# Optimization experiments

Measured on AMD Instinct MI355X. Metric: run time of the kernel, lower is better.

Reference implementation:

```python
import jax, jax.numpy as jnp
import numpy as np

LOG2 = 0.6931471805599453

def ssp(x):
    # shifted softplus: softplus(x) - log(2)
    return jax.nn.softplus(x) - LOG2

def residual(v, W, b):
    # PhysNetResidual reuses the same linear twice: linear(act(linear(act(x)))) + x
    h = ssp(v) @ W + b
    h = ssp(h) @ W + b
    return h + v

def setup_inputs() -> dict:
    key = jax.random.key(0)
    ks = jax.random.split(key, 20)
    N, E, D, R = 50000, 600000, 128, 32
    n_int, n_atom_res, n_out_res = 3, 1, 1
    def orth(k, shape):
        return jax.random.orthogonal(k, shape[0])[: shape[0], : shape[1]].astype(jnp.float32) if shape[0] == shape[1] else jax.random.normal(k, shape, jnp.float32) * (1.0 / np.sqrt(shape[0]))
    return {
        "x": jax.random.normal(ks[0], (N, D), jnp.float32),
        "g_ij": jax.random.uniform(ks[1], (E, R), jnp.float32),
        "Wf": orth(ks[2], (D, D)), "bf": jnp.zeros((D,), jnp.float32),
        "Wg": jax.random.normal(ks[3], (R, D), jnp.float32) * (1.0 / np.sqrt(R)),
        "Wj": orth(ks[4], (D, D)), "bj": jnp.zeros((D,), jnp.float32),
        "Wi": orth(ks[5], (D, D)), "bi": jnp.zeros((D,), jnp.float32),
        "u": jnp.ones((D,), jnp.float32),
        "rWint": jnp.stack([orth(ks[6 + i], (D, D)) for i in range(n_int)]),
        "rbint": jnp.zeros((n_int, D), jnp.float32),
        "rWatom": jnp.stack([orth(ks[10 + i], (D, D)) for i in range(n_atom_res)]),
        "rbatom": jnp.zeros((n_atom_res, D), jnp.float32),
        "rWout": jnp.stack([orth(ks[12 + i], (D, D)) for i in range(n_out_res)]),
        "rbout": jnp.zeros((n_out_res, D), jnp.float32),
        "idx_i": jax.random.randint(ks[14], (E,), 0, N, jnp.int32),
        "idx_j": jax.random.randint(ks[15], (E,), 0, N, jnp.int32),
        "n_atoms": N,
    }

def reference(x, g_ij, Wf, bf, Wg, Wj, bj, Wi, bi, u,
              rWint, rbint, rWatom, rbatom, rWout, rbout,
              idx_i, idx_j, n_atoms):
    # --- PhysNetInteraction ---
    xa = ssp(x)                                   # [N, D]
    x_j = xa[idx_j]                               # gather -> [E, D]
    xp = u * xa                                   # [N, D]
    vp = ssp(x_j @ Wj + bj) * (g_ij @ Wg)         # [E, D] RBF-gated messages
    vm = ssp(xa @ Wi + bi)                        # [N, D]
    v = jax.ops.segment_sum(vp, idx_i, num_segments=n_atoms) + vm
    for k in range(rWint.shape[0]):
        v = residual(v, rWint[k], rbint[k])
    v = ssp(v)
    h = xp + v @ Wf + bf                          # [N, D]
    # --- atomic residual stack ---
    for k in range(rWatom.shape[0]):
        h = residual(h, rWatom[k], rbatom[k])
    # --- PhysNetOutput ---
    o = h
    for k in range(rWout.shape[0]):
        o = residual(o, rWout[k], rbout[k])
    o = ssp(o)
    return (o, h)
```

## Files before the change

kernel.cpp:

```cpp
#include <hip/hip_runtime.h>
#include <stdint.h>

#define LOG2F 0.693147180559945f

typedef __attribute__((ext_vector_type(8))) short short8;
typedef __attribute__((ext_vector_type(4))) float f32x4;

__device__ __forceinline__ float ssp(float x){
  float t = __expf(-fabsf(x));
  return fmaxf(x, 0.0f) + __logf(1.0f + t) - LOG2F;
}

__device__ __forceinline__ uint32_t bf16rn(float x){
  uint32_t u = __float_as_uint(x);
  return (u + 0x7fffu + ((u >> 16) & 1u)) >> 16;
}
__device__ __forceinline__ void split2(float x, unsigned short &h, unsigned short &l){
  uint32_t hb = bf16rn(x);
  h = (unsigned short)hb;
  float hf = __uint_as_float(hb << 16);
  l = (unsigned short)bf16rn(x - hf);
}


__global__ __launch_bounds__(256) void k_xconv(
    const float* __restrict__ x, unsigned short* __restrict__ xs,
    float* __restrict__ vacc, int* __restrict__ cnt, int total)
{
  int i = (blockIdx.x * 256 + threadIdx.x) * 4;
  if (i >= total) return;
  int row = i >> 7, col = i & 127;
  float4 f4 = *(const float4*)(x + i);
  ushort4 h4, l4;
  split2(ssp(f4.x), h4.x, l4.x);
  split2(ssp(f4.y), h4.y, l4.y);
  split2(ssp(f4.z), h4.z, l4.z);
  split2(ssp(f4.w), h4.w, l4.w);
  *(ushort4*)(xs + (size_t)row * 256 + col)       = h4;
  *(ushort4*)(xs + (size_t)row * 256 + 128 + col) = l4;
  *(float4*)(vacc + i) = (float4){0.f, 0.f, 0.f, 0.f};
  if (col == 0) cnt[row] = 0;
}

__global__ __launch_bounds__(256) void k_wconv(
    const float* __restrict__ Wj, const float* __restrict__ Wg,
    const float* __restrict__ Wi, const float* __restrict__ Wf,
    const float* __restrict__ Wint, const float* __restrict__ Watm,
    const float* __restrict__ Wout,
    unsigned short* __restrict__ ws, int ni, int na, int no,
    const int* __restrict__ idx_i, int* __restrict__ cnt, int E)
{
  const int nmat = 3 + ni + na + no;
  int t = blockIdx.x * 256 + threadIdx.x;
  int m = t >> 11, r = t & 2047;
  if (m < nmat){
    const float* src;
    if      (m == 0)           src = Wj;
    else if (m == 1)           src = Wi;
    else if (m <= 1 + ni)      src = Wint + (size_t)(m - 2) * 16384;
    else if (m == 2 + ni)      src = Wf;
    else if (m <= 2 + ni + na) src = Watm + (size_t)(m - 3 - ni) * 16384;
    else                       src = Wout + (size_t)(m - 3 - ni - na) * 16384;
    int lane = r & 63, s = (r >> 6) & 3, ct = r >> 8;
    int col = ct * 16 + (lane & 15);
    int k0  = s * 32 + (lane >> 4) * 8;
    union { unsigned short u[8]; uint4 v; } H, L;
#pragma unroll
    for (int i = 0; i < 8; ++i) split2(src[(size_t)(k0 + i) * 128 + col], H.u[i], L.u[i]);
    ((uint4*)ws)[(size_t)m * 4096 + ((ct * 4 + s) * 2 + 0) * 64 + lane] = H.v;
    ((uint4*)ws)[(size_t)m * 4096 + ((ct * 4 + s) * 2 + 1) * 64 + lane] = L.v;
  } else {
    int uu = t - nmat * 2048;
    if (uu < 512){
      int lane = uu & 63, ct = uu >> 6;
      int col = ct * 16 + (lane & 15);
      int k0  = (lane >> 4) * 8;
      union { unsigned short u8[8]; uint4 v; } H, L;
#pragma unroll
      for (int i = 0; i < 8; ++i) split2(Wg[(size_t)(k0 + i) * 128 + col], H.u8[i], L.u8[i]);
      ((uint4*)ws)[(size_t)nmat * 4096 + (ct * 2 + 0) * 64 + lane] = H.v;
      ((uint4*)ws)[(size_t)nmat * 4096 + (ct * 2 + 1) * 64 + lane] = L.v;
    }
  }
  const int stride = gridDim.x * 256;
  for (int e = blockIdx.x * 256 + threadIdx.x; e < E; e += stride)
    atomicAdd(&cnt[idx_i[e]], 1);
}

__global__ __launch_bounds__(256) void k_scan1(
    int* __restrict__ cnt, int* __restrict__ bsums, int N)
{
  __shared__ int sh[256];
  const int t = threadIdx.x;
  const int base = blockIdx.x * 2048 + t * 8;
  int loc[8], s = 0;
#pragma unroll
  for (int k = 0; k < 8; ++k){
    int v = (base + k < N) ? cnt[base + k] : 0;
    loc[k] = s; s += v;
  }
  sh[t] = s;
  __syncthreads();
  const int own = s;
  for (int off = 1; off < 256; off <<= 1){
    int v = (t >= off) ? sh[t - off] : 0;
    __syncthreads();
    sh[t] += v;
    __syncthreads();
  }
  const int ex = sh[t] - own;
#pragma unroll
  for (int k = 0; k < 8; ++k)
    if (base + k < N) cnt[base + k] = ex + loc[k];
  if (t == 255) bsums[blockIdx.x] = sh[255];
}

__global__ void k_scan2(int* __restrict__ bsums, int nblk){
  if (threadIdx.x == 0 && blockIdx.x == 0){
    int run = 0;
    for (int b = 0; b < nblk; ++b){ int v = bsums[b]; bsums[b] = run; run += v; }
  }
}

__global__ __launch_bounds__(256) void k_scatter(
    const int* __restrict__ idx_i, int* __restrict__ cnt,
    const int* __restrict__ bsums, int* __restrict__ perm, int E)
{
  int e = blockIdx.x * 256 + threadIdx.x;
  if (e < E){
    int ii = idx_i[e];
    int p = atomicAdd(&cnt[ii], 1) + bsums[ii >> 11];
    perm[p] = e;
  }
}

__global__ __launch_bounds__(256) void k_edge(
    const unsigned short* __restrict__ xs, const float* __restrict__ g,
    const int* __restrict__ idx_i, const int* __restrict__ idx_j,
    const int* __restrict__ perm,
    const short8* __restrict__ wjf, const short8* __restrict__ wgf,
    const float* __restrict__ bj, float* vacc, int E)
{
  __shared__ __align__(16) char smem[16384 + 4096];
  short8* ahl = (short8*)smem;
  short8* ghl = (short8*)(smem + 16384);
  float*  vp_s = (float*)smem;
  __shared__ int ii_s[32];

  const int t    = threadIdx.x;
  const int lane = t & 63;
  const int w    = t >> 6;
  const int l15  = lane & 15;
  const int lq   = lane >> 4;
  const int e0   = blockIdx.x * 32;

  {
    const int row = t >> 3, kseg = t & 7;
    const int pe = e0 + row;
    const int e = (pe < E) ? perm[pe] : 0;
    const int j = idx_j[e];
    const short8* xp = (const short8*)(xs + (size_t)j * 256);
    const int q0 = kseg * 2;
    short8 fh0 = xp[q0    ];
    short8 fh1 = xp[q0 + 1];
    short8 fl0 = xp[16 + q0    ];
    short8 fl1 = xp[16 + q0 + 1];
    ahl[0*512 + (q0+0)*32 + (row ^ (q0+0))] = fh0;
    ahl[0*512 + (q0+1)*32 + (row ^ (q0+1))] = fh1;
    ahl[1*512 + (q0+0)*32 + (row ^ (q0+0))] = fl0;
    ahl[1*512 + (q0+1)*32 + (row ^ (q0+1))] = fl1;
  }
  if (t < 64){
    const int row = t >> 1, kseg = t & 1;
    const int pe = e0 + row;
    const int e = (pe < E) ? perm[pe] : 0;
    const float4* gp = (const float4*)(g + (size_t)e * 32 + kseg * 16);
    short8 fh0, fh1, fl0, fl1;
#pragma unroll
    for (int q = 0; q < 4; ++q){
      float4 f4 = gp[q];
      float vv[4] = {f4.x, f4.y, f4.z, f4.w};
#pragma unroll
      for (int uu = 0; uu < 4; ++uu){
        unsigned short hh, ll;
        split2(vv[uu], hh, ll);
        int i = q * 4 + uu;
        if (i < 8){ fh0[i]   = (short)hh; fl0[i]   = (short)ll; }
        else      { fh1[i-8] = (short)hh; fl1[i-8] = (short)ll; }
      }
    }
    const int q0 = kseg * 2;
    ghl[0*128 + (q0+0)*32 + (row ^ (q0+0))] = fh0;
    ghl[0*128 + (q0+1)*32 + (row ^ (q0+1))] = fh1;
    ghl[1*128 + (q0+0)*32 + (row ^ (q0+0))] = fl0;
    ghl[1*128 + (q0+1)*32 + (row ^ (q0+1))] = fl1;
  }
  if (t >= 64 && t < 96){
    int rr = t - 64, pe = e0 + rr;
    ii_s[rr] = (pe < E) ? idx_i[perm[pe]] : -1;
  }
  __syncthreads();

  f32x4 am[2][2], ag[2][2];
#pragma unroll
  for (int a = 0; a < 2; ++a)
#pragma unroll
    for (int b = 0; b < 2; ++b){
      am[a][b] = (f32x4){0.f, 0.f, 0.f, 0.f};
      ag[a][b] = (f32x4){0.f, 0.f, 0.f, 0.f};
    }

#pragma unroll
  for (int s = 0; s < 4; ++s){
    const int q = s * 4 + lq;
    short8 a0h = ahl[0*512 + q*32 + ((l15     ) ^ q)];
    short8 a0l = ahl[1*512 + q*32 + ((l15     ) ^ q)];
    short8 a1h = ahl[0*512 + q*32 + ((16 + l15) ^ q)];
    short8 a1l = ahl[1*512 + q*32 + ((16 + l15) ^ q)];
#pragma unroll
    for (int c = 0; c < 2; ++c){
      const int ct = w * 2 + c;
      short8 bh = wjf[((ct*4 + s)*2 + 0)*64 + lane];
      short8 bl = wjf[((ct*4 + s)*2 + 1)*64 + lane];
      am[0][c] = __builtin_amdgcn_mfma_f32_16x16x32_bf16(a0h, bh, am[0][c], 0, 0, 0);
      am[0][c] = __builtin_amdgcn_mfma_f32_16x16x32_bf16(a0h, bl, am[0][c], 0, 0, 0);
      am[0][c] = __builtin_amdgcn_mfma_f32_16x16x32_bf16(a0l, bh, am[0][c], 0, 0, 0);
      am[1][c] = __builtin_amdgcn_mfma_f32_16x16x32_bf16(a1h, bh, am[1][c], 0, 0, 0);
      am[1][c] = __builtin_amdgcn_mfma_f32_16x16x32_bf16(a1h, bl, am[1][c], 0, 0, 0);
      am[1][c] = __builtin_amdgcn_mfma_f32_16x16x32_bf16(a1l, bh, am[1][c], 0, 0, 0);
    }
  }
  {
    const int q = lq;
    short8 g0h = ghl[0*128 + q*32 + ((l15     ) ^ q)];
    short8 g0l = ghl[1*128 + q*32 + ((l15     ) ^ q)];
    short8 g1h = ghl[0*128 + q*32 + ((16 + l15) ^ q)];
    short8 g1l = ghl[1*128 + q*32 + ((16 + l15) ^ q)];
#pragma unroll
    for (int c = 0; c < 2; ++c){
      const int ct = w * 2 + c;
      short8 bh = wgf[(ct*2 + 0)*64 + lane];
      short8 bl = wgf[(ct*2 + 1)*64 + lane];
      ag[0][c] = __builtin_amdgcn_mfma_f32_16x16x32_bf16(g0h, bh, ag[0][c], 0, 0, 0);
      ag[0][c] = __builtin_amdgcn_mfma_f32_16x16x32_bf16(g0h, bl, ag[0][c], 0, 0, 0);
      ag[0][c] = __builtin_amdgcn_mfma_f32_16x16x32_bf16(g0l, bh, ag[0][c], 0, 0, 0);
      ag[1][c] = __builtin_amdgcn_mfma_f32_16x16x32_bf16(g1h, bh, ag[1][c], 0, 0, 0);
      ag[1][c] = __builtin_amdgcn_mfma_f32_16x16x32_bf16(g1h, bl, ag[1][c], 0, 0, 0);
      ag[1][c] = __builtin_amdgcn_mfma_f32_16x16x32_bf16(g1l, bh, ag[1][c], 0, 0, 0);
    }
  }

  __syncthreads();
#pragma unroll
  for (int c = 0; c < 2; ++c){
    const int col = (w * 2 + c) * 16 + l15;
    const float bjv = bj[col];
#pragma unroll
    for (int rt = 0; rt < 2; ++rt)
#pragma unroll
      for (int r = 0; r < 4; ++r){
        const int row = rt * 16 + lq * 4 + r;
        vp_s[col * 33 + row] = ssp(am[rt][c][r] + bjv) * ag[rt][c][r];
      }
  }
  __syncthreads();
  {
    const int col = t & 127;
    const int rbase = (t >> 7) * 16;
    float acc = 0.f;
    int curi = -1;
#pragma unroll
    for (int r = 0; r < 16; ++r){
      const int ii = ii_s[rbase + r];
      const float v = vp_s[col * 33 + rbase + r];
      if (ii == curi) acc += v;
      else {
        if (curi >= 0) atomicAdd(&vacc[(size_t)curi * 128 + col], acc);
        acc = v; curi = ii;
      }
    }
    if (curi >= 0) atomicAdd(&vacc[(size_t)curi * 128 + col], acc);
  }
}

__global__ __launch_bounds__(256) void k_chain(
    const float* __restrict__ x, const float* vacc,
    const short8* __restrict__ wcf,
    const float* __restrict__ bi, const float* __restrict__ bf_,
    const float* __restrict__ u,
    const float* __restrict__ bint, const float* __restrict__ batm,
    const float* __restrict__ bout,
    float* out, int N, int ni, int na, int no)
{
  __shared__ short8 ahl[2][1024];

  const int t    = threadIdx.x;
  const int lane = t & 63;
  const int w    = t >> 6;
  const int l15  = lane & 15;
  const int lq   = lane >> 4;
  const int r0   = blockIdx.x * 32;

  const int col0 = (w*2 + 0)*16 + l15;
  const int col1 = (w*2 + 1)*16 + l15;
  const int q0c = col0 >> 3, e0c = col0 & 7;
  const int q1c = col1 >> 3, e1c = col1 & 7;

  f32x4 am[2][2];
  int cur = 0;

  auto frag_put = [&](int b, int row, int qc, int ec, float v){
    unsigned short hh, ll;
    split2(v, hh, ll);
    unsigned short* base = (unsigned short*)&ahl[b][0];
    const int idx = (qc*32 + (row ^ qc))*8 + ec;
    base[idx]        = hh;
    base[4096 + idx] = ll;
  };

  auto gemm = [&](const short8* __restrict__ wf){
    const short8* A = &ahl[cur][0];
#pragma unroll
    for (int a = 0; a < 2; ++a)
#pragma unroll
      for (int b = 0; b < 2; ++b) am[a][b] = (f32x4){0.f, 0.f, 0.f, 0.f};
#pragma unroll
    for (int s = 0; s < 4; ++s){
      const int q = s * 4 + lq;
      short8 a0h = A[0*512 + q*32 + ((l15     ) ^ q)];
      short8 a0l = A[1*512 + q*32 + ((l15     ) ^ q)];
      short8 a1h = A[0*512 + q*32 + ((16 + l15) ^ q)];
      short8 a1l = A[1*512 + q*32 + ((16 + l15) ^ q)];
#pragma unroll
      for (int c = 0; c < 2; ++c){
        const int ct = w * 2 + c;
        short8 bh = wf[((ct*4 + s)*2 + 0)*64 + lane];
        short8 bl = wf[((ct*4 + s)*2 + 1)*64 + lane];
        am[0][c] = __builtin_amdgcn_mfma_f32_16x16x32_bf16(a0h, bh, am[0][c], 0, 0, 0);
        am[0][c] = __builtin_amdgcn_mfma_f32_16x16x32_bf16(a0h, bl, am[0][c], 0, 0, 0);
        am[0][c] = __builtin_amdgcn_mfma_f32_16x16x32_bf16(a0l, bh, am[0][c], 0, 0, 0);
        am[1][c] = __builtin_amdgcn_mfma_f32_16x16x32_bf16(a1h, bh, am[1][c], 0, 0, 0);
        am[1][c] = __builtin_amdgcn_mfma_f32_16x16x32_bf16(a1h, bl, am[1][c], 0, 0, 0);
        am[1][c] = __builtin_amdgcn_mfma_f32_16x16x32_bf16(a1l, bh, am[1][c], 0, 0, 0);
      }
    }
  };

  auto put_ssp_state = [&](float (&st)[2][2][4]){
    const int b = cur ^ 1;
#pragma unroll
    for (int rt = 0; rt < 2; ++rt)
#pragma unroll
      for (int r = 0; r < 4; ++r){
        const int row = rt*16 + lq*4 + r;
        frag_put(b, row, q0c, e0c, ssp(st[rt][0][r]));
        frag_put(b, row, q1c, e1c, ssp(st[rt][1][r]));
      }
    __syncthreads();
    cur = b;
  };
  auto put_ssp_amb = [&](float b0, float b1){
    const int b = cur ^ 1;
#pragma unroll
    for (int rt = 0; rt < 2; ++rt)
#pragma unroll
      for (int r = 0; r < 4; ++r){
        const int row = rt*16 + lq*4 + r;
        frag_put(b, row, q0c, e0c, ssp(am[rt][0][r] + b0));
        frag_put(b, row, q1c, e1c, ssp(am[rt][1][r] + b1));
      }
    __syncthreads();
    cur = b;
  };

  auto residual = [&](float (&st)[2][2][4], const short8* wf, const float* bvec){
    const float b0 = bvec[col0], b1 = bvec[col1];
    put_ssp_state(st);
    gemm(wf);
    put_ssp_amb(b0, b1);
    gemm(wf);
#pragma unroll
    for (int rt = 0; rt < 2; ++rt)
#pragma unroll
      for (int r = 0; r < 4; ++r){
        st[rt][0][r] += am[rt][0][r] + b0;
        st[rt][1][r] += am[rt][1][r] + b1;
      }
  };

  float xar[2][2][4];
#pragma unroll
  for (int rt = 0; rt < 2; ++rt)
#pragma unroll
    for (int r = 0; r < 4; ++r){
      int row = r0 + rt*16 + lq*4 + r; if (row >= N) row = N - 1;
      const int lrow = rt*16 + lq*4 + r;
      float v0 = ssp(x[(size_t)row*128 + col0]);
      float v1 = ssp(x[(size_t)row*128 + col1]);
      xar[rt][0][r] = v0; xar[rt][1][r] = v1;
      frag_put(0, lrow, q0c, e0c, v0);
      frag_put(0, lrow, q1c, e1c, v1);
    }
  __syncthreads();

  gemm(wcf + 0);
  float vst[2][2][4];
  {
    const float b0 = bi[col0], b1 = bi[col1];
#pragma unroll
    for (int rt = 0; rt < 2; ++rt)
#pragma unroll
      for (int r = 0; r < 4; ++r){
        int row = r0 + rt*16 + lq*4 + r; if (row >= N) row = N - 1;
        vst[rt][0][r] = vacc[(size_t)row*128 + col0] + ssp(am[rt][0][r] + b0);
        vst[rt][1][r] = vacc[(size_t)row*128 + col1] + ssp(am[rt][1][r] + b1);
      }
  }

  for (int kk = 0; kk < ni; ++kk)
    residual(vst, wcf + (size_t)(1 + kk) * 4096, bint + kk*128);

  put_ssp_state(vst);
  gemm(wcf + (size_t)(1 + ni) * 4096);
  float hst[2][2][4];
  {
    const float b0 = bf_[col0], b1 = bf_[col1];
    const float u0 = u[col0],   u1 = u[col1];
#pragma unroll
    for (int rt = 0; rt < 2; ++rt)
#pragma unroll
      for (int r = 0; r < 4; ++r){
        hst[rt][0][r] = u0 * xar[rt][0][r] + am[rt][0][r] + b0;
        hst[rt][1][r] = u1 * xar[rt][1][r] + am[rt][1][r] + b1;
      }
  }

  for (int kk = 0; kk < na; ++kk)
    residual(hst, wcf + (size_t)(2 + ni + kk) * 4096, batm + kk*128);

#pragma unroll
  for (int rt = 0; rt < 2; ++rt)
#pragma unroll
    for (int r = 0; r < 4; ++r){
      const int row = r0 + rt*16 + lq*4 + r;
      if (row < N){
        out[(size_t)N*128 + (size_t)row*128 + col0] = hst[rt][0][r];
        out[(size_t)N*128 + (size_t)row*128 + col1] = hst[rt][1][r];
      }
    }

  for (int kk = 0; kk < no; ++kk)
    residual(hst, wcf + (size_t)(2 + ni + na + kk) * 4096, bout + kk*128);

#pragma unroll
  for (int rt = 0; rt < 2; ++rt)
#pragma unroll
    for (int r = 0; r < 4; ++r){
      const int row = r0 + rt*16 + lq*4 + r;
      if (row < N){
        out[(size_t)row*128 + col0] = ssp(hst[rt][0][r]);
        out[(size_t)row*128 + col1] = ssp(hst[rt][1][r]);
      }
    }
}

extern "C" void kernel_launch(void* const* d_in, const int* in_sizes, int n_in,
                              void* d_out, int out_size, void* d_ws, size_t ws_size,
                              hipStream_t stream)
{
  const float* x    = (const float*)d_in[0];
  const float* g    = (const float*)d_in[1];
  const float* Wf   = (const float*)d_in[2];
  const float* bf_  = (const float*)d_in[3];
  const float* Wg   = (const float*)d_in[4];
  const float* Wj   = (const float*)d_in[5];
  const float* bj   = (const float*)d_in[6];
  const float* Wi   = (const float*)d_in[7];
  const float* bi   = (const float*)d_in[8];
  const float* u    = (const float*)d_in[9];
  const float* Wint = (const float*)d_in[10];
  const float* bint = (const float*)d_in[11];
  const float* Watm = (const float*)d_in[12];
  const float* batm = (const float*)d_in[13];
  const float* Wout = (const float*)d_in[14];
  const float* bout = (const float*)d_in[15];
  const int* idx_i  = (const int*)d_in[16];
  const int* idx_j  = (const int*)d_in[17];

  const int N  = in_sizes[0] / 128;
  const int E  = in_sizes[16];
  const int ni = in_sizes[10] / 16384;
  const int na = in_sizes[12] / 16384;
  const int no = in_sizes[14] / 16384;

  const int nmat = 3 + ni + na + no;

  float* vacc = (float*)d_out;
  short8* wsf = (short8*)d_ws;
  const short8* wjf = wsf;
  const short8* wcf = wsf + (size_t)1 * 4096;
  const short8* wgf = wsf + (size_t)nmat * 4096;

  const size_t frag_bytes = (size_t)(nmat + 1) * 65536;
  int* cnt   = (int*)((char*)d_ws + frag_bytes);
  int* bsums = cnt + N;
  int* perm  = bsums + 1024;
  char* after = (char*)(perm + E);
  const size_t used = (size_t)(after - (char*)d_ws);
  const size_t xs_bytes = (size_t)N * 256 * sizeof(unsigned short);
  unsigned short* xs = (ws_size >= used + xs_bytes)
      ? (unsigned short*)after
      : (unsigned short*)((float*)d_out + (size_t)N * 128);

  const int nblk = (N + 2047) / 2048;

  k_xconv  <<<dim3((N*128/4 + 255)/256), dim3(256), 0, stream>>>(x, xs, vacc, cnt, N * 128);
  k_wconv  <<<dim3((nmat + 1) * 8), dim3(256), 0, stream>>>(Wj, Wg, Wi, Wf, Wint, Watm, Wout,
                                                            (unsigned short*)d_ws, ni, na, no,
                                                            idx_i, cnt, E);
  k_scan1  <<<dim3(nblk), dim3(256), 0, stream>>>(cnt, bsums, N);
  k_scan2  <<<dim3(1), dim3(64), 0, stream>>>(bsums, nblk);
  k_scatter<<<dim3((E + 255)/256), dim3(256), 0, stream>>>(idx_i, cnt, bsums, perm, E);
  k_edge   <<<dim3((E + 31)/32), dim3(256), 0, stream>>>(xs, g, idx_i, idx_j, perm,
                                                         wjf, wgf, bj, vacc, E);
  k_chain  <<<dim3((N + 31)/32), dim3(256), 0, stream>>>(x, vacc, wcf,
                                                         bi, bf_, u, bint, batm, bout,
                                                         (float*)d_out, N, ni, na, no);
}
```

Baseline: 537.0 us.

## Pipeline edge gathers across four tiles per block and fold block-prefix scan into scatter

The edge kernel now handles 128 edges per block as four sequential 32-edge tiles. It loads the permuted indices up front and prefetches the next tile's gathered x rows into registers while the current tile is stored to LDS and computed, to hide gather latency. LDS buffers are no longer aliased, which raises LDS use per block and may lower occupancy; launch bounds request 4 blocks per CU. Separately, the single-thread k_scan2 launch is removed when there are at most 64 block sums: k_scatter computes the exclusive prefix itself with a wave shuffle scan.

```diff
diff --git a/kernel.cpp b/kernel.cpp
--- a/kernel.cpp
+++ b/kernel.cpp
@@ -124,162 +124,211 @@
 
 __global__ __launch_bounds__(256) void k_scatter(
     const int* __restrict__ idx_i, int* __restrict__ cnt,
-    const int* __restrict__ bsums, int* __restrict__ perm, int E)
-{
-  int e = blockIdx.x * 256 + threadIdx.x;
+    const int* __restrict__ bsums, int* __restrict__ perm, int E,
+    int nblk, int pref_in_kernel)
+{
+  __shared__ int spref[64];
+  const int t = threadIdx.x;
+  if (pref_in_kernel){
+    if (t < 64){
+      int v = (t < nblk) ? bsums[t] : 0;
+      int x = v;
+#pragma unroll
+      for (int off = 1; off < 64; off <<= 1){
+        int y = __shfl_up(x, off);
+        if (t >= off) x += y;
+      }
+      spref[t] = x - v;
+    }
+  } else {
+    if (t < 64) spref[t] = (t < nblk) ? bsums[t] : 0;
+  }
+  __syncthreads();
+  int e = blockIdx.x * 256 + t;
   if (e < E){
     int ii = idx_i[e];
-    int p = atomicAdd(&cnt[ii], 1) + bsums[ii >> 11];
+    int p = atomicAdd(&cnt[ii], 1) + spref[ii >> 11];
     perm[p] = e;
   }
 }
 
-__global__ __launch_bounds__(256) void k_edge(
+__global__ __launch_bounds__(256, 4) void k_edge(
     const unsigned short* __restrict__ xs, const float* __restrict__ g,
     const int* __restrict__ idx_i, const int* __restrict__ idx_j,
     const int* __restrict__ perm,
     const short8* __restrict__ wjf, const short8* __restrict__ wgf,
     const float* __restrict__ bj, float* vacc, int E)
 {
-  __shared__ __align__(16) char smem[16384 + 4096];
-  short8* ahl = (short8*)smem;
-  short8* ghl = (short8*)(smem + 16384);
-  float*  vp_s = (float*)smem;
-  __shared__ int ii_s[32];
+  __shared__ short8 ahl[1024];
+  __shared__ short8 ghl[256];
+  __shared__ float  vp_s[128*33];
+  __shared__ int    ii_s[32];
 
   const int t    = threadIdx.x;
   const int lane = t & 63;
   const int w    = t >> 6;
   const int l15  = lane & 15;
   const int lq   = lane >> 4;
-  const int e0   = blockIdx.x * 32;
-
+  const int ebase = blockIdx.x * 128;
+
+  const int rowA = t >> 3;
+  const int q0   = (t & 7) * 2;
+
+  const int colA = (w*2 + 0)*16 + l15;
+  const int colB = (w*2 + 1)*16 + l15;
+  const float bjA = bj[colA], bjB = bj[colB];
+
+  int jA[4] = {0,0,0,0}, egi[4] = {0,0,0,0}, iiv[4] = {-1,-1,-1,-1};
+#pragma unroll
+  for (int tt = 0; tt < 4; ++tt){
+    int pe = ebase + tt*32 + rowA;
+    int e = (pe < E) ? perm[pe] : 0;
+    jA[tt] = idx_j[e];
+  }
+  if (t < 64){
+    const int rowG = t >> 1;
+#pragma unroll
+    for (int tt = 0; tt < 4; ++tt){
+      int pe = ebase + tt*32 + rowG;
+      egi[tt] = (pe < E) ? perm[pe] : 0;
+    }
+  } else if (t < 96){
+    const int rr = t - 64;
+#pragma unroll
+    for (int tt = 0; tt < 4; ++tt){
+      int pe = ebase + tt*32 + rr;
+      iiv[tt] = (pe < E) ? idx_i[perm[pe]] : -1;
+    }
+  }
+
+  short8 A0a, A0b, A0c, A0d, A1a, A1b, A1c, A1d;
   {
-    const int row = t >> 3, kseg = t & 7;
-    const int pe = e0 + row;
-    const int e = (pe < E) ? perm[pe] : 0;
-    const int j = idx_j[e];
-    const short8* xp = (const short8*)(xs + (size_t)j * 256);
-    const int q0 = kseg * 2;
-    short8 fh0 = xp[q0    ];
-    short8 fh1 = xp[q0 + 1];
-    short8 fl0 = xp[16 + q0    ];
-    short8 fl1 = xp[16 + q0 + 1];
-    ahl[0*512 + (q0+0)*32 + (row ^ (q0+0))] = fh0;
-    ahl[0*512 + (q0+1)*32 + (row ^ (q0+1))] = fh1;
-    ahl[1*512 + (q0+0)*32 + (row ^ (q0+0))] = fl0;
-    ahl[1*512 + (q0+1)*32 + (row ^ (q0+1))] = fl1;
-  }
-  if (t < 64){
-    const int row = t >> 1, kseg = t & 1;
-    const int pe = e0 + row;
-    const int e = (pe < E) ? perm[pe] : 0;
-    const float4* gp = (const float4*)(g + (size_t)e * 32 + kseg * 16);
-    short8 fh0, fh1, fl0, fl1;
-#pragma unroll
-    for (int q = 0; q < 4; ++q){
-      float4 f4 = gp[q];
-      float vv[4] = {f4.x, f4.y, f4.z, f4.w};
-#pragma unroll
-      for (int uu = 0; uu < 4; ++uu){
-        unsigned short hh, ll;
-        split2(vv[uu], hh, ll);
-        int i = q * 4 + uu;
-        if (i < 8){ fh0[i]   = (short)hh; fl0[i]   = (short)ll; }
-        else      { fh1[i-8] = (short)hh; fl1[i-8] = (short)ll; }
-      }
-    }
-    const int q0 = kseg * 2;
-    ghl[0*128 + (q0+0)*32 + (row ^ (q0+0))] = fh0;
-    ghl[0*128 + (q0+1)*32 + (row ^ (q0+1))] = fh1;
-    ghl[1*128 + (q0+0)*32 + (row ^ (q0+0))] = fl0;
-    ghl[1*128 + (q0+1)*32 + (row ^ (q0+1))] = fl1;
-  }
-  if (t >= 64 && t < 96){
-    int rr = t - 64, pe = e0 + rr;
-    ii_s[rr] = (pe < E) ? idx_i[perm[pe]] : -1;
-  }
-  __syncthreads();
-
-  f32x4 am[2][2], ag[2][2];
-#pragma unroll
-  for (int a = 0; a < 2; ++a)
-#pragma unroll
-    for (int b = 0; b < 2; ++b){
-      am[a][b] = (f32x4){0.f, 0.f, 0.f, 0.f};
-      ag[a][b] = (f32x4){0.f, 0.f, 0.f, 0.f};
-    }
-
-#pragma unroll
-  for (int s = 0; s < 4; ++s){
-    const int q = s * 4 + lq;
-    short8 a0h = ahl[0*512 + q*32 + ((l15     ) ^ q)];
-    short8 a0l = ahl[1*512 + q*32 + ((l15     ) ^ q)];
-    short8 a1h = ahl[0*512 + q*32 + ((16 + l15) ^ q)];
-    short8 a1l = ahl[1*512 + q*32 + ((16 + l15) ^ q)];
+    const short8* xp = (const short8*)(xs + (size_t)jA[0] * 256);
+    A0a = xp[q0]; A0b = xp[q0+1]; A0c = xp[16+q0]; A0d = xp[16+q0+1];
+  }
+
+#pragma unroll
+  for (int tt = 0; tt < 4; ++tt){
+    {
+      short8 ca, cb, cc, cd;
+      if ((tt & 1) == 0){ ca=A0a; cb=A0b; cc=A0c; cd=A0d; }
+      else              { ca=A1a; cb=A1b; cc=A1c; cd=A1d; }
+      ahl[0*512 + (q0+0)*32 + (rowA ^ (q0+0))] = ca;
+      ahl[0*512 + (q0+1)*32 + (rowA ^ (q0+1))] = cb;
+      ahl[1*512 + (q0+0)*32 + (rowA ^ (q0+0))] = cc;
+      ahl[1*512 + (q0+1)*32 + (rowA ^ (q0+1))] = cd;
+    }
+    if (tt < 3){
+      const short8* xp = (const short8*)(xs + (size_t)jA[tt+1] * 256);
+      if ((tt & 1) == 0){ A1a=xp[q0]; A1b=xp[q0+1]; A1c=xp[16+q0]; A1d=xp[16+q0+1]; }
+      else              { A0a=xp[q0]; A0b=xp[q0+1]; A0c=xp[16+q0]; A0d=xp[16+q0+1]; }
+    }
+    if (t < 64){
+      const int rowG = t >> 1, qg0 = (t & 1) * 2;
+      const float4* gp = (const float4*)(g + (size_t)egi[tt] * 32 + (t & 1) * 16);
+      float4 f0 = gp[0], f1 = gp[1], f2 = gp[2], f3 = gp[3];
+      float vv[16] = {f0.x,f0.y,f0.z,f0.w, f1.x,f1.y,f1.z,f1.w,
+                      f2.x,f2.y,f2.z,f2.w, f3.x,f3.y,f3.z,f3.w};
+      short8 fh0, fh1, fl0, fl1;
+#pragma unroll
+      for (int i2 = 0; i2 < 8; ++i2){
+        unsigned short hh, ll; split2(vv[i2], hh, ll);
+        fh0[i2] = (short)hh; fl0[i2] = (short)ll;
+      }
+#pragma unroll
+      for (int i2 = 0; i2 < 8; ++i2){
+        unsigned short hh, ll; split2(vv[8+i2], hh, ll);
+        fh1[i2] = (short)hh; fl1[i2] = (short)ll;
+      }
+      ghl[0*128 + (qg0+0)*32 + (rowG ^ (qg0+0))] = fh0;
+      ghl[0*128 + (qg0+1)*32 + (rowG ^ (qg0+1))] = fh1;
+      ghl[1*128 + (qg0+0)*32 + (rowG ^ (qg0+0))] = fl0;
+      ghl[1*128 + (qg0+1)*32 + (rowG ^ (qg0+1))] = fl1;
+    } else if (t < 96){
+      ii_s[t - 64] = iiv[tt];
+    }
+    __syncthreads();
+
+    f32x4 am[2][2], ag[2][2];
+#pragma unroll
+    for (int a = 0; a < 2; ++a)
+#pragma unroll
+      for (int b = 0; b < 2; ++b){
+        am[a][b] = (f32x4){0.f, 0.f, 0.f, 0.f};
+        ag[a][b] = (f32x4){0.f, 0.f, 0.f, 0.f};
+      }
+
+#pragma unroll
+    for (int s = 0; s < 4; ++s){
+      const int q = s * 4 + lq;
+      short8 a0h = ahl[0*512 + q*32 + ((l15     ) ^ q)];
+      short8 a0l = ahl[1*512 + q*32 + ((l15     ) ^ q)];
+      short8 a1h = ahl[0*512 + q*32 + ((16 + l15) ^ q)];
+      short8 a1l = ahl[1*512 + q*32 + ((16 + l15) ^ q)];
+#pragma unroll
+      for (int c = 0; c < 2; ++c){
+        const int ct = w * 2 + c;
+        short8 bh = wjf[((ct*4 + s)*2 + 0)*64 + lane];
+        short8 bl = wjf[((ct*4 + s)*2 + 1)*64 + lane];
+        am[0][c] = __builtin_amdgcn_mfma_f32_16x16x32_bf16(a0h, bh, am[0][c], 0, 0, 0);
+        am[0][c] = __builtin_amdgcn_mfma_f32_16x16x32_bf16(a0h, bl, am[0][c], 0, 0, 0);
+        am[0][c] = __builtin_amdgcn_mfma_f32_16x16x32_bf16(a0l, bh, am[0][c], 0, 0, 0);
+        am[1][c] = __builtin_amdgcn_mfma_f32_16x16x32_bf16(a1h, bh, am[1][c], 0, 0, 0);
+        am[1][c] = __builtin_amdgcn_mfma_f32_16x16x32_bf16(a1h, bl, am[1][c], 0, 0, 0);
+        am[1][c] = __builtin_amdgcn_mfma_f32_16x16x32_bf16(a1l, bh, am[1][c], 0, 0, 0);
+      }
+    }
+    {
+      const int q = lq;
+      short8 g0h = ghl[0*128 + q*32 + ((l15     ) ^ q)];
+      short8 g0l = ghl[1*128 + q*32 + ((l15     ) ^ q)];
+      short8 g1h = ghl[0*128 + q*32 + ((16 + l15) ^ q)];
+      short8 g1l = ghl[1*128 + q*32 + ((16 + l15) ^ q)];
+#pragma unroll
+      for (int c = 0; c < 2; ++c){
+        const int ct = w * 2 + c;
+        short8 bh = wgf[(ct*2 + 0)*64 + lane];
+        short8 bl = wgf[(ct*2 + 1)*64 + lane];
+        ag[0][c] = __builtin_amdgcn_mfma_f32_16x16x32_bf16(g0h, bh, ag[0][c], 0, 0, 0);
+        ag[0][c] = __builtin_amdgcn_mfma_f32_16x16x32_bf16(g0h, bl, ag[0][c], 0, 0, 0);
+        ag[0][c] = __builtin_amdgcn_mfma_f32_16x16x32_bf16(g0l, bh, ag[0][c], 0, 0, 0);
+        ag[1][c] = __builtin_amdgcn_mfma_f32_16x16x32_bf16(g1h, bh, ag[1][c], 0, 0, 0);
+        ag[1][c] = __builtin_amdgcn_mfma_f32_16x16x32_bf16(g1h, bl, ag[1][c], 0, 0, 0);
+        ag[1][c] = __builtin_amdgcn_mfma_f32_16x16x32_bf16(g1l, bh, ag[1][c], 0, 0, 0);
+      }
+    }
+
 #pragma unroll
     for (int c = 0; c < 2; ++c){
-      const int ct = w * 2 + c;
-      short8 bh = wjf[((ct*4 + s)*2 + 0)*64 + lane];
-      short8 bl = wjf[((ct*4 + s)*2 + 1)*64 + lane];
-      am[0][c] = __builtin_amdgcn_mfma_f32_16x16x32_bf16(a0h, bh, am[0][c], 0, 0, 0);
-      am[0][c] = __builtin_amdgcn_mfma_f32_16x16x32_bf16(a0h, bl, am[0][c], 0, 0, 0);
-      am[0][c] = __builtin_amdgcn_mfma_f32_16x16x32_bf16(a0l, bh, am[0][c], 0, 0, 0);
-      am[1][c] = __builtin_amdgcn_mfma_f32_16x16x32_bf16(a1h, bh, am[1][c], 0, 0, 0);
-      am[1][c] = __builtin_amdgcn_mfma_f32_16x16x32_bf16(a1h, bl, am[1][c], 0, 0, 0);
-      am[1][c] = __builtin_amdgcn_mfma_f32_16x16x32_bf16(a1l, bh, am[1][c], 0, 0, 0);
-    }
-  }
-  {
-    const int q = lq;
-    short8 g0h = ghl[0*128 + q*32 + ((l15     ) ^ q)];
-    short8 g0l = ghl[1*128 + q*32 + ((l15     ) ^ q)];
-    short8 g1h = ghl[0*128 + q*32 + ((16 + l15) ^ q)];
-    short8 g1l = ghl[1*128 + q*32 + ((16 + l15) ^ q)];
-#pragma unroll
-    for (int c = 0; c < 2; ++c){
-      const int ct = w * 2 + c;
-      short8 bh = wgf[(ct*2 + 0)*64 + lane];
-      short8 bl = wgf[(ct*2 + 1)*64 + lane];
-      ag[0][c] = __builtin_amdgcn_mfma_f32_16x16x32_bf16(g0h, bh, ag[0][c], 0, 0, 0);
-      ag[0][c] = __builtin_amdgcn_mfma_f32_16x16x32_bf16(g0h, bl, ag[0][c], 0, 0, 0);
-      ag[0][c] = __builtin_amdgcn_mfma_f32_16x16x32_bf16(g0l, bh, ag[0][c], 0, 0, 0);
-      ag[1][c] = __builtin_amdgcn_mfma_f32_16x16x32_bf16(g1h, bh, ag[1][c], 0, 0, 0);
-      ag[1][c] = __builtin_amdgcn_mfma_f32_16x16x32_bf16(g1h, bl, ag[1][c], 0, 0, 0);
-      ag[1][c] = __builtin_amdgcn_mfma_f32_16x16x32_bf16(g1l, bh, ag[1][c], 0, 0, 0);
-    }
-  }
-
-  __syncthreads();
-#pragma unroll
-  for (int c = 0; c < 2; ++c){
-    const int col = (w * 2 + c) * 16 + l15;
-    const float bjv = bj[col];
-#pragma unroll
-    for (int rt = 0; rt < 2; ++rt)
-#pragma unroll
-      for (int r = 0; r < 4; ++r){
-        const int row = rt * 16 + lq * 4 + r;
-        vp_s[col * 33 + row] = ssp(am[rt][c][r] + bjv) * ag[rt][c][r];
-      }
-  }
-  __syncthreads();
-  {
-    const int col = t & 127;
-    const int rbase = (t >> 7) * 16;
-    float acc = 0.f;
-    int curi = -1;
-#pragma unroll
-    for (int r = 0; r < 16; ++r){
-      const int ii = ii_s[rbase + r];
-      const float v = vp_s[col * 33 + rbase + r];
-      if (ii == curi) acc += v;
-      else {
-        if (curi >= 0) atomicAdd(&vacc[(size_t)curi * 128 + col], acc);
-        acc = v; curi = ii;
-      }
-    }
-    if (curi >= 0) atomicAdd(&vacc[(size_t)curi * 128 + col], acc);
+      const int col = (c == 0) ? colA : colB;
+      const float bjv = (c == 0) ? bjA : bjB;
+#pragma unroll
+      for (int rt = 0; rt < 2; ++rt)
+#pragma unroll
+        for (int r = 0; r < 4; ++r){
+          const int row = rt * 16 + lq * 4 + r;
+          vp_s[col * 33 + row] = ssp(am[rt][c][r] + bjv) * ag[rt][c][r];
+        }
+    }
+    __syncthreads();
+    {
+      const int col = t & 127;
+      const int rbase = (t >> 7) * 16;
+      float acc = 0.f;
+      int curi = -1;
+#pragma unroll
+      for (int r = 0; r < 16; ++r){
+        const int ii = ii_s[rbase + r];
+        const float v = vp_s[col * 33 + rbase + r];
+        if (ii == curi) acc += v;
+        else {
+          if (curi >= 0) atomicAdd(&vacc[(size_t)curi * 128 + col], acc);
+          acc = v; curi = ii;
+        }
+      }
+      if (curi >= 0) atomicAdd(&vacc[(size_t)curi * 128 + col], acc);
+    }
+    __syncthreads();
   }
 }
 
@@ -513,16 +562,19 @@
       : (unsigned short*)((float*)d_out + (size_t)N * 128);
 
   const int nblk = (N + 2047) / 2048;
+  const int pref_fold = (nblk <= 64) ? 1 : 0;
 
   k_xconv  <<<dim3((N*128/4 + 255)/256), dim3(256), 0, stream>>>(x, xs, vacc, cnt, N * 128);
   k_wconv  <<<dim3((nmat + 1) * 8), dim3(256), 0, stream>>>(Wj, Wg, Wi, Wf, Wint, Watm, Wout,
                                                             (unsigned short*)d_ws, ni, na, no,
                                                             idx_i, cnt, E);
   k_scan1  <<<dim3(nblk), dim3(256), 0, stream>>>(cnt, bsums, N);
-  k_scan2  <<<dim3(1), dim3(64), 0, stream>>>(bsums, nblk);
-  k_scatter<<<dim3((E + 255)/256), dim3(256), 0, stream>>>(idx_i, cnt, bsums, perm, E);
-  k_edge   <<<dim3((E + 31)/32), dim3(256), 0, stream>>>(xs, g, idx_i, idx_j, perm,
-                                                         wjf, wgf, bj, vacc, E);
+  if (!pref_fold)
+    k_scan2<<<dim3(1), dim3(64), 0, stream>>>(bsums, nblk);
+  k_scatter<<<dim3((E + 255)/256), dim3(256), 0, stream>>>(idx_i, cnt, bsums, perm, E,
+                                                           nblk, pref_fold);
+  k_edge   <<<dim3((E + 127)/128), dim3(256), 0, stream>>>(xs, g, idx_i, idx_j, perm,
+                                                           wjf, wgf, bj, vacc, E);
   k_chain  <<<dim3((N + 31)/32), dim3(256), 0, stream>>>(x, vacc, wcf,
                                                          bi, bf_, u, bint, batm, bout,
                                                          (float*)d_out, N, ni, na, no);
```

Measured after the change: 545.5 us. No clear change (+1.6%).
